# Optimization experiments

Hardware: AMD Instinct MI355X
Metric: run time of the kernel (lower is better)

## Reference

```python
import jax, jax.numpy as jnp
import numpy as np

B, C, H, W = 8, 512, 32, 32
NUM_HEADS = 8
HEAD_DIM = C // NUM_HEADS


def setup_inputs() -> dict:
    key = jax.random.key(0)
    k1, k2, k3 = jax.random.split(key, 3)
    s = 0.02
    return {
        "x": jax.random.normal(k1, (B, C, H, W), dtype=jnp.float32),
        "W_qkv": jax.random.normal(k2, (3 * C, C), dtype=jnp.float32) * s,
        "b_qkv": jnp.zeros((3 * C,), dtype=jnp.float32),
        "W_proj": jax.random.normal(k3, (C, C), dtype=jnp.float32) * s,
        "b_proj": jnp.zeros((C,), dtype=jnp.float32),
    }


def reference(x, W_qkv, b_qkv, W_proj, b_proj):
    b, c, h, w = x.shape
    n = h * w  # seq_len in raster order
    nh, hd = NUM_HEADS, c // NUM_HEADS
    scale = hd ** -0.5

    # b c h w -> b n c
    x_seq = x.reshape(b, c, n).transpose(0, 2, 1)
    qkv = x_seq @ W_qkv.T + b_qkv  # (b, n, 3c)
    # b n (3 nh hd) -> 3, b, nh, n, hd
    qkv = qkv.reshape(b, n, 3, nh, hd).transpose(2, 0, 3, 1, 4)
    q, k, v = qkv[0], qkv[1], qkv[2]

    attn = jnp.einsum('bhnd,bhmd->bhnm', q, k) * scale
    causal = jnp.tril(jnp.ones((n, n), dtype=bool))
    attn = jnp.where(causal, attn, -jnp.inf)
    attn = jax.nn.softmax(attn, axis=-1)

    out = jnp.einsum('bhnm,bhmd->bhnd', attn, v)
    out = out.transpose(0, 2, 1, 3).reshape(b, n, c)  # b n c
    out = out @ W_proj.T + b_proj
    # b (h w) c -> b c h w
    return out.transpose(0, 2, 1).reshape(b, c, h, w)
```

## Files before the change

### kernel.cpp

```cpp
#include <hip/hip_runtime.h>
#include <hip/hip_bf16.h>
#include <math.h>

#define B_  8
#define C_  512
#define N_  1024
#define NH_ 8
#define HD_ 64
#define C3_ 1536

typedef __bf16 bf16x8 __attribute__((ext_vector_type(8)));
typedef float  f32x4  __attribute__((ext_vector_type(4)));
typedef __hip_bfloat16 bf16;

__device__ __forceinline__ f32x4 mfma16(const bf16x8& a, const bf16x8& b, const f32x4& c) {
    return __builtin_amdgcn_mfma_f32_16x16x32_bf16(a, b, c, 0, 0, 0);
}

__device__ __forceinline__ void ld_lds16(const bf16* g, bf16* l_uniform) {
    __builtin_amdgcn_global_load_lds(
        (const __attribute__((address_space(1))) void*)(uintptr_t)g,
        (__attribute__((address_space(3))) void*)(uintptr_t)l_uniform,
        16, 0, 0);
}


__global__ __launch_bounds__(256) void cvt_w(const float* __restrict__ Wq,
                                             const float* __restrict__ Wp,
                                             bf16* __restrict__ Wqb,
                                             bf16* __restrict__ Wpb) {
    int i = blockIdx.x * 256 + threadIdx.x;
    if (i < C3_ * C_) Wqb[i] = __float2bfloat16(Wq[i]);
    else {
        int j = i - C3_ * C_;
        if (j < C_ * C_) Wpb[j] = __float2bfloat16(Wp[j]);
    }
}

__global__ __launch_bounds__(256) void transpose_x(const float* __restrict__ x,
                                                   bf16* __restrict__ xb) {
    __shared__ float T[32][33];
    const int n0 = blockIdx.x * 32, c0 = blockIdx.y * 32, b = blockIdx.z;
    const int tx = threadIdx.x, ty = threadIdx.y;
    const float* xp = x + ((size_t)b * C_ + c0) * N_ + n0;
#pragma unroll
    for (int l = 0; l < 4; ++l)
        T[ty + 8 * l][tx] = xp[(ty + 8 * l) * N_ + tx];
    __syncthreads();
    bf16* xo = xb + ((size_t)b * N_ + n0) * C_ + c0;
#pragma unroll
    for (int l = 0; l < 4; ++l)
        xo[(ty + 8 * l) * C_ + tx] = __float2bfloat16(T[tx][ty + 8 * l]);
}

__global__ __launch_bounds__(256) void qkv_mfma(const bf16* __restrict__ xb,
                                                const bf16* __restrict__ Wqb,
                                                const float* __restrict__ bq,
                                                bf16* __restrict__ Qb,
                                                bf16* __restrict__ Kb,
                                                bf16* __restrict__ Vt) {
    __shared__ bf16 As[128 * 32];
    __shared__ bf16 Bs[128 * 32];
    __shared__ bf16 Vl[4][16][20];
    const int tid = threadIdx.x, w = tid >> 6, lane = tid & 63;
    const int lo = lane & 15, hi = lane >> 4;
    const int j0 = blockIdx.x * 128;
    const int m0 = blockIdx.y * 128;
    const int b  = m0 >> 10;

    const int srow = w * 32 + (lane >> 2);
    const int scol = (lane & 3) * 8;
    const bf16* gA = xb  + (size_t)(m0 + srow) * C_ + scol;
    const bf16* gB = Wqb + (size_t)(j0 + srow) * C_ + scol;
    bf16* lA = As + (w * 32) * 32;
    bf16* lB = Bs + (w * 32) * 32;

    f32x4 acc[4][4];
#pragma unroll
    for (int mt = 0; mt < 4; ++mt)
#pragma unroll
        for (int jt = 0; jt < 4; ++jt)
            acc[mt][jt] = (f32x4){0.f, 0.f, 0.f, 0.f};

    for (int k0 = 0; k0 < C_; k0 += 32) {
        ld_lds16(gA + k0, lA);
        ld_lds16(gA + (size_t)16 * C_ + k0, lA + 16 * 32);
        ld_lds16(gB + k0, lB);
        ld_lds16(gB + (size_t)16 * C_ + k0, lB + 16 * 32);
        __syncthreads();

        bf16x8 af[4], bfr[4];
#pragma unroll
        for (int mt = 0; mt < 4; ++mt)
            af[mt] = *(const bf16x8*)(As + ((w & 1) * 64 + mt * 16 + lo) * 32 + hi * 8);
#pragma unroll
        for (int jt = 0; jt < 4; ++jt)
            bfr[jt] = *(const bf16x8*)(Bs + ((w >> 1) * 64 + jt * 16 + lo) * 32 + hi * 8);
#pragma unroll
        for (int mt = 0; mt < 4; ++mt)
#pragma unroll
            for (int jt = 0; jt < 4; ++jt)
                acc[mt][jt] = mfma16(af[mt], bfr[jt], acc[mt][jt]);
        __syncthreads();
    }

    const int jb = (w >> 1) * 64;
    const int nbase = (m0 & 1023) + (w & 1) * 64;
#pragma unroll
    for (int jt = 0; jt < 4; ++jt) {
        const int j16 = j0 + jb + jt * 16;
        const float bias = bq[j16 + lo];
        if (j16 < 512) {
            const int h = j16 >> 6, d = (j16 & 63) + lo;
            bf16* qp = Qb + ((size_t)(b * NH_ + h) * N_) * HD_ + d;
#pragma unroll
            for (int mt = 0; mt < 4; ++mt)
#pragma unroll
                for (int r = 0; r < 4; ++r) {
                    int n = nbase + mt * 16 + hi * 4 + r;
                    qp[(size_t)n * HD_] = __float2bfloat16((acc[mt][jt][r] + bias) * 0.125f);
                }
        } else if (j16 < 1024) {
            const int jj = j16 - 512;
            const int h = jj >> 6, d = (jj & 63) + lo;
            bf16* kp = Kb + ((size_t)(b * NH_ + h) * N_) * HD_ + d;
#pragma unroll
            for (int mt = 0; mt < 4; ++mt)
#pragma unroll
                for (int r = 0; r < 4; ++r) {
                    int n = nbase + mt * 16 + hi * 4 + r;
                    kp[(size_t)n * HD_] = __float2bfloat16(acc[mt][jt][r] + bias);
                }
        } else {
            const int jj = j16 - 1024;
            const int h = jj >> 6, dbase = jj & 63;
            bf16* vp = Vt + ((size_t)(b * NH_ + h) * HD_ + dbase) * N_ + nbase;
#pragma unroll
            for (int mt = 0; mt < 4; ++mt) {
#pragma unroll
                for (int r = 0; r < 4; ++r)
                    Vl[w][hi * 4 + r][lo] = __float2bfloat16(acc[mt][jt][r] + bias);
#pragma unroll
                for (int r = 0; r < 4; ++r)
                    vp[(size_t)(hi * 4 + r) * N_ + mt * 16 + lo] = Vl[w][lo][hi * 4 + r];
            }
        }
    }
}


__global__ __launch_bounds__(256) void attn_mfma(const bf16* __restrict__ Qb,
                                                 const bf16* __restrict__ Kb,
                                                 const bf16* __restrict__ Vt,
                                                 bf16* __restrict__ ao) {
    __shared__ __align__(16) bf16 Pl[4][2][2][16][40];

    const int wv   = threadIdx.x >> 6;
    const int lane = threadIdx.x & 63;
    const int lo   = lane & 15;
    const int hi   = lane >> 4;
    const int bh   = blockIdx.x & 63;
    const int pi   = (blockIdx.x >> 6) * 4 + wv;
    const int qwA  = pi * 16;
    const int qwB  = (63 - pi) * 16;

    const bf16* Qh = Qb + (size_t)bh * N_ * HD_;
    const bf16* Kh = Kb + (size_t)bh * N_ * HD_;
    const bf16* Vh = Vt + (size_t)bh * HD_ * N_;

    const bf16x8 qA0 = *(const bf16x8*)(Qh + (qwA + lo) * HD_ + hi * 8);
    const bf16x8 qA1 = *(const bf16x8*)(Qh + (qwA + lo) * HD_ + 32 + hi * 8);
    const bf16x8 qB0 = *(const bf16x8*)(Qh + (qwB + lo) * HD_ + hi * 8);
    const bf16x8 qB1 = *(const bf16x8*)(Qh + (qwB + lo) * HD_ + 32 + hi * 8);

    f32x4 OA[4], OB[4];
    float LA[4], LB[4];
#pragma unroll
    for (int r = 0; r < 4; ++r) {
        OA[0][r] = OA[1][r] = OA[2][r] = OA[3][r] = 0.f;
        OB[0][r] = OB[1][r] = OB[2][r] = OB[3][r] = 0.f;
        LA[r] = 0.f; LB[r] = 0.f;
    }

    const int nkbA = (qwA + 79) >> 6;
    const int nkbB = (qwB + 79) >> 6;

    for (int kb = 0; kb < nkbB; ++kb) {
        const int key0 = kb * 64;
        const bool doA = (kb < nkbA);

        bf16x8 kf[4][2];
#pragma unroll
        for (int t = 0; t < 4; ++t) {
            const bf16* kp = Kh + (size_t)(key0 + t * 16 + lo) * HD_ + hi * 8;
            kf[t][0] = *(const bf16x8*)(kp);
            kf[t][1] = *(const bf16x8*)(kp + 32);
        }
        bf16x8 vf[4][2];
#pragma unroll
        for (int t = 0; t < 4; ++t) {
            const bf16* vp = Vh + (size_t)(t * 16 + lo) * N_ + key0 + hi * 8;
            vf[t][0] = *(const bf16x8*)(vp);
            vf[t][1] = *(const bf16x8*)(vp + 32);
        }

        f32x4 SB[4], SA[4];
#pragma unroll
        for (int t = 0; t < 4; ++t) {
            SB[t] = (f32x4){0.f, 0.f, 0.f, 0.f};
            SB[t] = mfma16(qB0, kf[t][0], SB[t]);
            SB[t] = mfma16(qB1, kf[t][1], SB[t]);
        }
        if (doA) {
#pragma unroll
            for (int t = 0; t < 4; ++t) {
                SA[t] = (f32x4){0.f, 0.f, 0.f, 0.f};
                SA[t] = mfma16(qA0, kf[t][0], SA[t]);
                SA[t] = mfma16(qA1, kf[t][1], SA[t]);
            }
        }

        if (key0 + 63 > qwB) {
#pragma unroll
            for (int t = 0; t < 4; ++t)
#pragma unroll
                for (int r = 0; r < 4; ++r)
                    if (key0 + t * 16 + lo > qwB + hi * 4 + r) SB[t][r] = -1e30f;
        }
        if (doA && key0 + 63 > qwA) {
#pragma unroll
            for (int t = 0; t < 4; ++t)
#pragma unroll
                for (int r = 0; r < 4; ++r)
                    if (key0 + t * 16 + lo > qwA + hi * 4 + r) SA[t][r] = -1e30f;
        }

#pragma unroll
        for (int t = 0; t < 4; ++t)
#pragma unroll
            for (int r = 0; r < 4; ++r) {
                float p = __expf(SB[t][r]);
                LB[r] += p;
                Pl[wv][1][t >> 1][hi * 4 + r][(t & 1) * 16 + lo] = __float2bfloat16(p);
            }
        if (doA) {
#pragma unroll
            for (int t = 0; t < 4; ++t)
#pragma unroll
                for (int r = 0; r < 4; ++r) {
                    float p = __expf(SA[t][r]);
                    LA[r] += p;
                    Pl[wv][0][t >> 1][hi * 4 + r][(t & 1) * 16 + lo] = __float2bfloat16(p);
                }
        }

        bf16x8 paB0 = *(const bf16x8*)(&Pl[wv][1][0][lo][hi * 8]);
        bf16x8 paB1 = *(const bf16x8*)(&Pl[wv][1][1][lo][hi * 8]);
#pragma unroll
        for (int t = 0; t < 4; ++t) {
            OB[t] = mfma16(paB0, vf[t][0], OB[t]);
            OB[t] = mfma16(paB1, vf[t][1], OB[t]);
        }
        if (doA) {
            bf16x8 paA0 = *(const bf16x8*)(&Pl[wv][0][0][lo][hi * 8]);
            bf16x8 paA1 = *(const bf16x8*)(&Pl[wv][0][1][lo][hi * 8]);
#pragma unroll
            for (int t = 0; t < 4; ++t) {
                OA[t] = mfma16(paA0, vf[t][0], OA[t]);
                OA[t] = mfma16(paA1, vf[t][1], OA[t]);
            }
        }
    }

    const int b = bh >> 3, h = bh & 7;
#pragma unroll
    for (int c = 0; c < 2; ++c) {
        const int qw = c ? qwB : qwA;
        f32x4* O = c ? OB : OA;
        float* Lp = c ? LB : LA;
        float rL[4];
#pragma unroll
        for (int r = 0; r < 4; ++r) {
            float Ls = Lp[r];
#pragma unroll
            for (int off = 1; off < 16; off <<= 1)
                Ls += __shfl_xor(Ls, off, 64);
            rL[r] = 1.f / Ls;
        }
#pragma unroll
        for (int t = 0; t < 4; ++t)
#pragma unroll
            for (int r = 0; r < 4; ++r) {
                int q = qw + hi * 4 + r;
                ao[((size_t)b * N_ + q) * C_ + h * HD_ + t * 16 + lo] =
                    __float2bfloat16(O[t][r] * rL[r]);
            }
    }
}

__global__ __launch_bounds__(256) void proj_mfma(const bf16* __restrict__ aob,
                                                 const bf16* __restrict__ Wpb,
                                                 const float* __restrict__ bp,
                                                 float* __restrict__ out) {
    __shared__ bf16 As[64 * 32];
    __shared__ bf16 Bs[128 * 32];
    const int tid = threadIdx.x, w = tid >> 6, lane = tid & 63;
    const int lo = lane & 15, hi = lane >> 4;
    const int j0 = blockIdx.x * 64;
    const int n0 = blockIdx.y * 128;
    const int b  = n0 >> 10;

    const int r4 = lane >> 2, c8 = (lane & 3) * 8;
    const bf16* gA = Wpb + (size_t)(j0 + w * 16 + r4) * C_ + c8;
    const bf16* gB = aob + (size_t)(n0 + w * 32 + r4) * C_ + c8;
    bf16* lA = As + (w * 16) * 32;
    bf16* lB = Bs + (w * 32) * 32;

    f32x4 acc[2][4];
#pragma unroll
    for (int mt = 0; mt < 2; ++mt)
#pragma unroll
        for (int jt = 0; jt < 4; ++jt)
            acc[mt][jt] = (f32x4){0.f, 0.f, 0.f, 0.f};

    for (int k0 = 0; k0 < C_; k0 += 32) {
        ld_lds16(gA + k0, lA);
        ld_lds16(gB + k0, lB);
        ld_lds16(gB + (size_t)16 * C_ + k0, lB + 16 * 32);
        __syncthreads();

        bf16x8 af[2], bfr[4];
#pragma unroll
        for (int mt = 0; mt < 2; ++mt)
            af[mt] = *(const bf16x8*)(As + ((w & 1) * 32 + mt * 16 + lo) * 32 + hi * 8);
#pragma unroll
        for (int jt = 0; jt < 4; ++jt)
            bfr[jt] = *(const bf16x8*)(Bs + ((w >> 1) * 64 + jt * 16 + lo) * 32 + hi * 8);
#pragma unroll
        for (int mt = 0; mt < 2; ++mt)
#pragma unroll
            for (int jt = 0; jt < 4; ++jt)
                acc[mt][jt] = mfma16(af[mt], bfr[jt], acc[mt][jt]);
        __syncthreads();
    }

#pragma unroll
    for (int mt = 0; mt < 2; ++mt)
#pragma unroll
        for (int r = 0; r < 4; ++r) {
            const int j = j0 + (w & 1) * 32 + mt * 16 + hi * 4 + r;
            const float bias = bp[j];
            float* op = out + ((size_t)(b * C_ + j)) * N_ + (n0 & 1023) + (w >> 1) * 64 + lo;
#pragma unroll
            for (int jt = 0; jt < 4; ++jt)
                op[jt * 16] = acc[mt][jt][r] + bias;
        }
}

extern "C" void kernel_launch(void* const* d_in, const int* in_sizes, int n_in,
                              void* d_out, int out_size, void* d_ws, size_t ws_size,
                              hipStream_t stream) {
    const float* x  = (const float*)d_in[0];
    const float* Wq = (const float*)d_in[1];
    const float* bq = (const float*)d_in[2];
    const float* Wp = (const float*)d_in[3];
    const float* bp = (const float*)d_in[4];
    float* out = (float*)d_out;

    const size_t headElems = (size_t)B_ * NH_ * N_ * HD_;
    bf16* xb  = (bf16*)d_ws;
    bf16* Wqb = xb + (size_t)B_ * N_ * C_;
    bf16* Wpb = Wqb + (size_t)C3_ * C_;
    bf16* Qb  = Wpb + (size_t)C_ * C_;
    bf16* Kb  = Qb + headElems;
    bf16* Vt  = Kb + headElems;
    bf16* aob = Vt + headElems;

    cvt_w<<<dim3((C3_ * C_ + C_ * C_ + 255) / 256), dim3(256), 0, stream>>>(Wq, Wp, Wqb, Wpb);
    transpose_x<<<dim3(N_ / 32, C_ / 32, B_), dim3(32, 8), 0, stream>>>(x, xb);

    qkv_mfma<<<dim3(C3_ / 128, (B_ * N_) / 128), dim3(256), 0, stream>>>(xb, Wqb, bq, Qb, Kb, Vt);
    attn_mfma<<<dim3(8 * 64), dim3(256), 0, stream>>>(Qb, Kb, Vt, aob);
    proj_mfma<<<dim3(C_ / 64, (B_ * N_) / 128), dim3(256), 0, stream>>>(aob, Wpb, bp, out);
}
```

Baseline: 169.9 us.

## Compute transposed scores so P feeds PV MFMA from registers, dropping LDS round-trip

```diff
diff --git a/kernel.cpp b/kernel.cpp
--- a/kernel.cpp
+++ b/kernel.cpp
@@ -9,12 +9,19 @@
 #define HD_ 64
 #define C3_ 1536
 
-typedef __bf16 bf16x8 __attribute__((ext_vector_type(8)));
-typedef float  f32x4  __attribute__((ext_vector_type(4)));
+typedef __bf16 bf16x8  __attribute__((ext_vector_type(8)));
+typedef __bf16 bf16x4v __attribute__((ext_vector_type(4)));
+typedef short  s16x4   __attribute__((ext_vector_type(4)));
+typedef float  f32x4   __attribute__((ext_vector_type(4)));
 typedef __hip_bfloat16 bf16;
 
 __device__ __forceinline__ f32x4 mfma16(const bf16x8& a, const bf16x8& b, const f32x4& c) {
     return __builtin_amdgcn_mfma_f32_16x16x32_bf16(a, b, c, 0, 0, 0);
+}
+
+__device__ __forceinline__ f32x4 mfma_pv(const bf16x4v& a, const bf16x4v& b, const f32x4& c) {
+    return __builtin_amdgcn_mfma_f32_16x16x16bf16_1k(
+        __builtin_bit_cast(s16x4, a), __builtin_bit_cast(s16x4, b), c, 0, 0, 0);
 }
 
 __device__ __forceinline__ void ld_lds16(const bf16* g, bf16* l_uniform) {
@@ -153,8 +160,7 @@
                                                  const bf16* __restrict__ Kb,
                                                  const bf16* __restrict__ Vt,
                                                  bf16* __restrict__ ao) {
-    __shared__ __align__(16) bf16 Pl[4][2][2][16][40];
-
+    __shared__ __bf16 Ot[4][16][72];
     const int wv   = threadIdx.x >> 6;
     const int lane = threadIdx.x & 63;
     const int lo   = lane & 15;
@@ -174,12 +180,11 @@
     const bf16x8 qB1 = *(const bf16x8*)(Qh + (qwB + lo) * HD_ + 32 + hi * 8);
 
     f32x4 OA[4], OB[4];
-    float LA[4], LB[4];
-#pragma unroll
-    for (int r = 0; r < 4; ++r) {
-        OA[0][r] = OA[1][r] = OA[2][r] = OA[3][r] = 0.f;
-        OB[0][r] = OB[1][r] = OB[2][r] = OB[3][r] = 0.f;
-        LA[r] = 0.f; LB[r] = 0.f;
+    float LAc = 0.f, LBc = 0.f;
+#pragma unroll
+    for (int t = 0; t < 4; ++t) {
+        OA[t] = (f32x4){0.f, 0.f, 0.f, 0.f};
+        OB[t] = (f32x4){0.f, 0.f, 0.f, 0.f};
     }
 
     const int nkbA = (qwA + 79) >> 6;
@@ -196,27 +201,28 @@
             kf[t][0] = *(const bf16x8*)(kp);
             kf[t][1] = *(const bf16x8*)(kp + 32);
         }
-        bf16x8 vf[4][2];
+        bf16x4v vf[4][4];
 #pragma unroll
         for (int t = 0; t < 4; ++t) {
-            const bf16* vp = Vh + (size_t)(t * 16 + lo) * N_ + key0 + hi * 8;
-            vf[t][0] = *(const bf16x8*)(vp);
-            vf[t][1] = *(const bf16x8*)(vp + 32);
+            const bf16* vp = Vh + (size_t)(t * 16 + lo) * N_ + key0 + 4 * hi;
+#pragma unroll
+            for (int s = 0; s < 4; ++s)
+                vf[t][s] = *(const bf16x4v*)(vp + s * 16);
         }
 
         f32x4 SB[4], SA[4];
 #pragma unroll
         for (int t = 0; t < 4; ++t) {
             SB[t] = (f32x4){0.f, 0.f, 0.f, 0.f};
-            SB[t] = mfma16(qB0, kf[t][0], SB[t]);
-            SB[t] = mfma16(qB1, kf[t][1], SB[t]);
+            SB[t] = mfma16(kf[t][0], qB0, SB[t]);
+            SB[t] = mfma16(kf[t][1], qB1, SB[t]);
         }
         if (doA) {
 #pragma unroll
             for (int t = 0; t < 4; ++t) {
                 SA[t] = (f32x4){0.f, 0.f, 0.f, 0.f};
-                SA[t] = mfma16(qA0, kf[t][0], SA[t]);
-                SA[t] = mfma16(qA1, kf[t][1], SA[t]);
+                SA[t] = mfma16(kf[t][0], qA0, SA[t]);
+                SA[t] = mfma16(kf[t][1], qA1, SA[t]);
             }
         }
 
@@ -225,23 +231,24 @@
             for (int t = 0; t < 4; ++t)
 #pragma unroll
                 for (int r = 0; r < 4; ++r)
-                    if (key0 + t * 16 + lo > qwB + hi * 4 + r) SB[t][r] = -1e30f;
+                    if (key0 + t * 16 + 4 * hi + r > qwB + lo) SB[t][r] = -1e30f;
         }
         if (doA && key0 + 63 > qwA) {
 #pragma unroll
             for (int t = 0; t < 4; ++t)
 #pragma unroll
                 for (int r = 0; r < 4; ++r)
-                    if (key0 + t * 16 + lo > qwA + hi * 4 + r) SA[t][r] = -1e30f;
-        }
-
+                    if (key0 + t * 16 + 4 * hi + r > qwA + lo) SA[t][r] = -1e30f;
+        }
+
+        bf16x4v pB[4], pA[4];
 #pragma unroll
         for (int t = 0; t < 4; ++t)
 #pragma unroll
             for (int r = 0; r < 4; ++r) {
                 float p = __expf(SB[t][r]);
-                LB[r] += p;
-                Pl[wv][1][t >> 1][hi * 4 + r][(t & 1) * 16 + lo] = __float2bfloat16(p);
+                LBc += p;
+                pB[t][r] = (__bf16)p;
             }
         if (doA) {
 #pragma unroll
@@ -249,26 +256,22 @@
 #pragma unroll
                 for (int r = 0; r < 4; ++r) {
                     float p = __expf(SA[t][r]);
-                    LA[r] += p;
-                    Pl[wv][0][t >> 1][hi * 4 + r][(t & 1) * 16 + lo] = __float2bfloat16(p);
+                    LAc += p;
+                    pA[t][r] = (__bf16)p;
                 }
         }
 
-        bf16x8 paB0 = *(const bf16x8*)(&Pl[wv][1][0][lo][hi * 8]);
-        bf16x8 paB1 = *(const bf16x8*)(&Pl[wv][1][1][lo][hi * 8]);
-#pragma unroll
-        for (int t = 0; t < 4; ++t) {
-            OB[t] = mfma16(paB0, vf[t][0], OB[t]);
-            OB[t] = mfma16(paB1, vf[t][1], OB[t]);
-        }
+#pragma unroll
+        for (int t = 0; t < 4; ++t)
+#pragma unroll
+            for (int s = 0; s < 4; ++s)
+                OB[t] = mfma_pv(vf[t][s], pB[s], OB[t]);
         if (doA) {
-            bf16x8 paA0 = *(const bf16x8*)(&Pl[wv][0][0][lo][hi * 8]);
-            bf16x8 paA1 = *(const bf16x8*)(&Pl[wv][0][1][lo][hi * 8]);
-#pragma unroll
-            for (int t = 0; t < 4; ++t) {
-                OA[t] = mfma16(paA0, vf[t][0], OA[t]);
-                OA[t] = mfma16(paA1, vf[t][1], OA[t]);
-            }
+#pragma unroll
+            for (int t = 0; t < 4; ++t)
+#pragma unroll
+                for (int s = 0; s < 4; ++s)
+                    OA[t] = mfma_pv(vf[t][s], pA[s], OA[t]);
         }
     }
 
@@ -277,24 +280,21 @@
     for (int c = 0; c < 2; ++c) {
         const int qw = c ? qwB : qwA;
         f32x4* O = c ? OB : OA;
-        float* Lp = c ? LB : LA;
-        float rL[4];
-#pragma unroll
-        for (int r = 0; r < 4; ++r) {
-            float Ls = Lp[r];
-#pragma unroll
-            for (int off = 1; off < 16; off <<= 1)
-                Ls += __shfl_xor(Ls, off, 64);
-            rL[r] = 1.f / Ls;
-        }
+        float Lc = c ? LBc : LAc;
+        Lc += __shfl_xor(Lc, 16, 64);
+        Lc += __shfl_xor(Lc, 32, 64);
+        const float rL = 1.f / Lc;
 #pragma unroll
         for (int t = 0; t < 4; ++t)
 #pragma unroll
-            for (int r = 0; r < 4; ++r) {
-                int q = qw + hi * 4 + r;
-                ao[((size_t)b * N_ + q) * C_ + h * HD_ + t * 16 + lo] =
-                    __float2bfloat16(O[t][r] * rL[r]);
-            }
+            for (int r = 0; r < 4; ++r)
+                Ot[wv][lo][t * 16 + 4 * hi + r] = (__bf16)(O[t][r] * rL);
+#pragma unroll
+        for (int p = 0; p < 4; ++p) {
+            const int q = p * 4 + hi;
+            bf16x4v o4 = *(const bf16x4v*)(&Ot[wv][q][lo * 4]);
+            *(bf16x4v*)(ao + ((size_t)b * N_ + qw + q) * C_ + h * HD_ + lo * 4) = o4;
+        }
     }
 }
 
```

Measured after the change: 192.7 us. +13.4%, slower.

## Stage K/V tiles in shared LDS via global_load_lds across block waves

Applied to the files above, without the earlier changes.

```diff
diff --git a/kernel.cpp b/kernel.cpp
--- a/kernel.cpp
+++ b/kernel.cpp
@@ -153,14 +153,18 @@
                                                  const bf16* __restrict__ Kb,
                                                  const bf16* __restrict__ Vt,
                                                  bf16* __restrict__ ao) {
+    __shared__ bf16 Ks0[64 * 32], Ks1[64 * 32];
+    __shared__ bf16 Vs0[64 * 32], Vs1[64 * 32];
     __shared__ __align__(16) bf16 Pl[4][2][2][16][40];
 
-    const int wv   = threadIdx.x >> 6;
-    const int lane = threadIdx.x & 63;
+    const int tid  = threadIdx.x;
+    const int wv   = tid >> 6;
+    const int lane = tid & 63;
     const int lo   = lane & 15;
     const int hi   = lane >> 4;
     const int bh   = blockIdx.x & 63;
-    const int pi   = (blockIdx.x >> 6) * 4 + wv;
+    const int blk  = blockIdx.x >> 6;
+    const int pi   = blk * 4 + wv;
     const int qwA  = pi * 16;
     const int qwB  = (63 - pi) * 16;
 
@@ -173,6 +177,15 @@
     const bf16x8 qB0 = *(const bf16x8*)(Qh + (qwB + lo) * HD_ + hi * 8);
     const bf16x8 qB1 = *(const bf16x8*)(Qh + (qwB + lo) * HD_ + 32 + hi * 8);
 
+    const int srow = tid >> 2;
+    const int scol = (tid & 3) * 8;
+    const bf16* gK = Kh + (size_t)srow * HD_ + scol;
+    const bf16* gV = Vh + (size_t)srow * N_ + scol;
+    bf16* lK0 = Ks0 + wv * 512;
+    bf16* lK1 = Ks1 + wv * 512;
+    bf16* lV0 = Vs0 + wv * 512;
+    bf16* lV1 = Vs1 + wv * 512;
+
     f32x4 OA[4], OB[4];
     float LA[4], LB[4];
 #pragma unroll
@@ -182,94 +195,99 @@
         LA[r] = 0.f; LB[r] = 0.f;
     }
 
-    const int nkbA = (qwA + 79) >> 6;
-    const int nkbB = (qwB + 79) >> 6;
-
-    for (int kb = 0; kb < nkbB; ++kb) {
+    const int nkbA   = (qwA + 79) >> 6;
+    const int nkbB   = (qwB + 79) >> 6;
+    const int nkbBlk = ((63 - blk * 4) * 16 + 79) >> 6;
+
+    for (int kb = 0; kb < nkbBlk; ++kb) {
         const int key0 = kb * 64;
-        const bool doA = (kb < nkbA);
-
-        bf16x8 kf[4][2];
-#pragma unroll
-        for (int t = 0; t < 4; ++t) {
-            const bf16* kp = Kh + (size_t)(key0 + t * 16 + lo) * HD_ + hi * 8;
-            kf[t][0] = *(const bf16x8*)(kp);
-            kf[t][1] = *(const bf16x8*)(kp + 32);
+
+        ld_lds16(gK + (size_t)key0 * HD_,      lK0);
+        ld_lds16(gK + (size_t)key0 * HD_ + 32, lK1);
+        ld_lds16(gV + key0,                    lV0);
+        ld_lds16(gV + key0 + 32,               lV1);
+        __syncthreads();
+
+        if (kb < nkbB) {
+            const bool doA = (kb < nkbA);
+
+            bf16x8 kf[4][2], vf[4][2];
+#pragma unroll
+            for (int t = 0; t < 4; ++t) {
+                kf[t][0] = *(const bf16x8*)(Ks0 + (t * 16 + lo) * 32 + hi * 8);
+                kf[t][1] = *(const bf16x8*)(Ks1 + (t * 16 + lo) * 32 + hi * 8);
+                vf[t][0] = *(const bf16x8*)(Vs0 + (t * 16 + lo) * 32 + hi * 8);
+                vf[t][1] = *(const bf16x8*)(Vs1 + (t * 16 + lo) * 32 + hi * 8);
+            }
+
+            f32x4 SB[4], SA[4];
+#pragma unroll
+            for (int t = 0; t < 4; ++t) {
+                SB[t] = (f32x4){0.f, 0.f, 0.f, 0.f};
+                SB[t] = mfma16(qB0, kf[t][0], SB[t]);
+                SB[t] = mfma16(qB1, kf[t][1], SB[t]);
+            }
+            if (doA) {
+#pragma unroll
+                for (int t = 0; t < 4; ++t) {
+                    SA[t] = (f32x4){0.f, 0.f, 0.f, 0.f};
+                    SA[t] = mfma16(qA0, kf[t][0], SA[t]);
+                    SA[t] = mfma16(qA1, kf[t][1], SA[t]);
+                }
+            }
+
+            if (key0 + 63 > qwB) {
+#pragma unroll
+                for (int t = 0; t < 4; ++t)
+#pragma unroll
+                    for (int r = 0; r < 4; ++r)
+                        if (key0 + t * 16 + lo > qwB + hi * 4 + r) SB[t][r] = -1e30f;
+            }
+            if (doA && key0 + 63 > qwA) {
+#pragma unroll
+                for (int t = 0; t < 4; ++t)
+#pragma unroll
+                    for (int r = 0; r < 4; ++r)
+                        if (key0 + t * 16 + lo > qwA + hi * 4 + r) SA[t][r] = -1e30f;
+            }
+
+#pragma unroll
+            for (int t = 0; t < 4; ++t)
+#pragma unroll
+                for (int r = 0; r < 4; ++r) {
+                    float p = __expf(SB[t][r]);
+                    LB[r] += p;
+                    Pl[wv][1][t >> 1][hi * 4 + r][(t & 1) * 16 + lo] = __float2bfloat16(p);
+                }
+            if (doA) {
+#pragma unroll
+                for (int t = 0; t < 4; ++t)
+#pragma unroll
+                    for (int r = 0; r < 4; ++r) {
+                        float p = __expf(SA[t][r]);
+                        LA[r] += p;
+                        Pl[wv][0][t >> 1][hi * 4 + r][(t & 1) * 16 + lo] = __float2bfloat16(p);
+                    }
+            }
+
+            bf16x8 paB0 = *(const bf16x8*)(&Pl[wv][1][0][lo][hi * 8]);
+            bf16x8 paB1 = *(const bf16x8*)(&Pl[wv][1][1][lo][hi * 8]);
+#pragma unroll
+            for (int t = 0; t < 4; ++t) {
+                OB[t] = mfma16(paB0, vf[t][0], OB[t]);
+                OB[t] = mfma16(paB1, vf[t][1], OB[t]);
+            }
+            if (doA) {
+                bf16x8 paA0 = *(const bf16x8*)(&Pl[wv][0][0][lo][hi * 8]);
+                bf16x8 paA1 = *(const bf16x8*)(&Pl[wv][0][1][lo][hi * 8]);
+#pragma unroll
+                for (int t = 0; t < 4; ++t) {
+                    OA[t] = mfma16(paA0, vf[t][0], OA[t]);
+                    OA[t] = mfma16(paA1, vf[t][1], OA[t]);
+                }
+            }
         }
-        bf16x8 vf[4][2];
-#pragma unroll
-        for (int t = 0; t < 4; ++t) {
-            const bf16* vp = Vh + (size_t)(t * 16 + lo) * N_ + key0 + hi * 8;
-            vf[t][0] = *(const bf16x8*)(vp);
-            vf[t][1] = *(const bf16x8*)(vp + 32);
-        }
-
-        f32x4 SB[4], SA[4];
-#pragma unroll
-        for (int t = 0; t < 4; ++t) {
-            SB[t] = (f32x4){0.f, 0.f, 0.f, 0.f};
-            SB[t] = mfma16(qB0, kf[t][0], SB[t]);
-            SB[t] = mfma16(qB1, kf[t][1], SB[t]);
-        }
-        if (doA) {
-#pragma unroll
-            for (int t = 0; t < 4; ++t) {
-                SA[t] = (f32x4){0.f, 0.f, 0.f, 0.f};
-                SA[t] = mfma16(qA0, kf[t][0], SA[t]);
-                SA[t] = mfma16(qA1, kf[t][1], SA[t]);
-            }
-        }
-
-        if (key0 + 63 > qwB) {
-#pragma unroll
-            for (int t = 0; t < 4; ++t)
-#pragma unroll
-                for (int r = 0; r < 4; ++r)
-                    if (key0 + t * 16 + lo > qwB + hi * 4 + r) SB[t][r] = -1e30f;
-        }
-        if (doA && key0 + 63 > qwA) {
-#pragma unroll
-            for (int t = 0; t < 4; ++t)
-#pragma unroll
-                for (int r = 0; r < 4; ++r)
-                    if (key0 + t * 16 + lo > qwA + hi * 4 + r) SA[t][r] = -1e30f;
-        }
-
-#pragma unroll
-        for (int t = 0; t < 4; ++t)
-#pragma unroll
-            for (int r = 0; r < 4; ++r) {
-                float p = __expf(SB[t][r]);
-                LB[r] += p;
-                Pl[wv][1][t >> 1][hi * 4 + r][(t & 1) * 16 + lo] = __float2bfloat16(p);
-            }
-        if (doA) {
-#pragma unroll
-            for (int t = 0; t < 4; ++t)
-#pragma unroll
-                for (int r = 0; r < 4; ++r) {
-                    float p = __expf(SA[t][r]);
-                    LA[r] += p;
-                    Pl[wv][0][t >> 1][hi * 4 + r][(t & 1) * 16 + lo] = __float2bfloat16(p);
-                }
-        }
-
-        bf16x8 paB0 = *(const bf16x8*)(&Pl[wv][1][0][lo][hi * 8]);
-        bf16x8 paB1 = *(const bf16x8*)(&Pl[wv][1][1][lo][hi * 8]);
-#pragma unroll
-        for (int t = 0; t < 4; ++t) {
-            OB[t] = mfma16(paB0, vf[t][0], OB[t]);
-            OB[t] = mfma16(paB1, vf[t][1], OB[t]);
-        }
-        if (doA) {
-            bf16x8 paA0 = *(const bf16x8*)(&Pl[wv][0][0][lo][hi * 8]);
-            bf16x8 paA1 = *(const bf16x8*)(&Pl[wv][0][1][lo][hi * 8]);
-#pragma unroll
-            for (int t = 0; t < 4; ++t) {
-                OA[t] = mfma16(paA0, vf[t][0], OA[t]);
-                OA[t] = mfma16(paA1, vf[t][1], OA[t]);
-            }
-        }
+        __syncthreads();
     }
 
     const int b = bh >> 3, h = bh & 7;
```

Result: faster. 142.4 us (-16.2%).
